# Kernel optimization log

Hardware: AMD Instinct MI355X
Metric: run time of the kernel (lower is better)

The kernel has to match this reference:

```python
import jax, jax.numpy as jnp
import numpy as np

N_NODES = 50000
E_EDGES = 800000
NEG_SLOPE = 0.2  # PyG GATConv LeakyReLU slope
BN_EPS = 1e-5


def _gat(x, src, dst, W, a_s, a_d, b, heads, ch, concat):
    """One GATConv (PyG semantics, eval mode): gather, per-edge attention,
    segment softmax over destination neighborhoods, scatter-add aggregation."""
    n = x.shape[0]
    h = (x @ W).reshape(n, heads, ch)                      # [N,H,C]
    es = jnp.sum(h * a_s, axis=-1)                         # [N,H] alpha_src per node
    ed = jnp.sum(h * a_d, axis=-1)                         # [N,H] alpha_dst per node
    e = jax.nn.leaky_relu(es[src] + ed[dst], NEG_SLOPE)    # [E,H] edge logits
    m = jax.ops.segment_max(e, dst, num_segments=n)        # stable segment softmax
    ex = jnp.exp(e - m[dst])
    den = jax.ops.segment_sum(ex, dst, num_segments=n)
    alpha = ex / den[dst]                                  # [E,H]
    out = jax.ops.segment_sum(h[src] * alpha[:, :, None], dst, num_segments=n)  # [N,H,C]
    out = out.reshape(n, heads * ch) if concat else out.mean(axis=1)
    return out + b


def _bn(x, g, b):
    # eval-mode BatchNorm1d with running_mean=0, running_var=1
    return x * (g / jnp.sqrt(1.0 + BN_EPS)) + b


def setup_inputs() -> dict:
    key = jax.random.key(0)
    k = jax.random.split(key, 24)
    s = 0.1
    inp = {
        "x": jax.random.normal(k[0], (N_NODES, 9), jnp.float32),
        "edge_index": jax.random.randint(k[1], (2, E_EDGES), 0, N_NODES, jnp.int32),
        "W1": jax.random.normal(k[2], (9, 512), jnp.float32) * s,
        "a1s": jax.random.normal(k[3], (8, 64), jnp.float32) * s,
        "a1d": jax.random.normal(k[4], (8, 64), jnp.float32) * s,
        "b1": jax.random.normal(k[5], (512,), jnp.float32) * s,
        "W2": jax.random.normal(k[6], (512, 128), jnp.float32) * s,
        "a2s": jax.random.normal(k[7], (4, 32), jnp.float32) * s,
        "a2d": jax.random.normal(k[8], (4, 32), jnp.float32) * s,
        "b2": jax.random.normal(k[9], (128,), jnp.float32) * s,
        "W3": jax.random.normal(k[10], (128, 32), jnp.float32) * s,
        "a3s": jax.random.normal(k[11], (1, 32), jnp.float32) * s,
        "a3d": jax.random.normal(k[12], (1, 32), jnp.float32) * s,
        "b3": jax.random.normal(k[13], (32,), jnp.float32) * s,
        "g1": jax.random.uniform(k[14], (512,), jnp.float32, 0.5, 1.5),
        "be1": jax.random.normal(k[15], (512,), jnp.float32) * s,
        "g2": jax.random.uniform(k[16], (128,), jnp.float32, 0.5, 1.5),
        "be2": jax.random.normal(k[17], (128,), jnp.float32) * s,
        "g3": jax.random.uniform(k[18], (32,), jnp.float32, 0.5, 1.5),
        "be3": jax.random.normal(k[19], (32,), jnp.float32) * s,
        "Wh": jax.random.normal(k[20], (32, 1), jnp.float32) * s,
        "bh": jax.random.normal(k[21], (1,), jnp.float32) * s,
    }
    return inp


def reference(x, edge_index, W1, a1s, a1d, b1, W2, a2s, a2d, b2,
              W3, a3s, a3d, b3, g1, be1, g2, be2, g3, be3, Wh, bh):
    n = x.shape[0]
    loops = jnp.arange(n, dtype=edge_index.dtype)          # PyG add_self_loops=True
    src = jnp.concatenate([edge_index[0], loops])
    dst = jnp.concatenate([edge_index[1], loops])
    h = _gat(x, src, dst, W1, a1s, a1d, b1, heads=8, ch=64, concat=True)
    h = jax.nn.elu(_bn(h, g1, be1))
    h = _gat(h, src, dst, W2, a2s, a2d, b2, heads=4, ch=32, concat=True)
    h = jax.nn.elu(_bn(h, g2, be2))
    h = _gat(h, src, dst, W3, a3s, a3d, b3, heads=1, ch=32, concat=False)
    h = jax.nn.elu(_bn(h, g3, be3))
    return h @ Wh + bh                                     # [N,1]
```

## Files before the change

### kernel.cpp

```cpp
#include <hip/hip_runtime.h>
#include <hip/hip_bf16.h>
#include <math.h>

#define N_NODES 50000
#define E_EDGES 800000
#define ET (E_EDGES + N_NODES)
#define NBLK_SCAN ((N_NODES + 255) / 256)
#define MPAD 50048
#define NPB_T1 16

typedef __attribute__((ext_vector_type(8))) short bf16x8;
typedef __attribute__((ext_vector_type(4))) float f32x4;
typedef __attribute__((ext_vector_type(8))) _Float16 half8;


__global__ void zero_int_kernel(int* __restrict__ p, int n) {
    int i = blockIdx.x * blockDim.x + threadIdx.x;
    if (i < n) p[i] = 0;
}

__global__ void hist_kernel(const int* __restrict__ ei, int* __restrict__ cnt) {
    int e = blockIdx.x * blockDim.x + threadIdx.x;
    if (e < ET) {
        int d = (e < E_EDGES) ? ei[E_EDGES + e] : (e - E_EDGES);
        atomicAdd(&cnt[d], 1);
    }
}

__global__ void scan1_kernel(const int* __restrict__ cnt, int* __restrict__ rp,
                             int* __restrict__ bsum) {
    __shared__ int s[256];
    int i = blockIdx.x * 256 + threadIdx.x;
    int v = (i < N_NODES) ? cnt[i] : 0;
    s[threadIdx.x] = v;
    __syncthreads();
    for (int off = 1; off < 256; off <<= 1) {
        int t = (threadIdx.x >= off) ? s[threadIdx.x - off] : 0;
        __syncthreads();
        s[threadIdx.x] += t;
        __syncthreads();
    }
    if (i < N_NODES) rp[i + 1] = s[threadIdx.x];
    if (threadIdx.x == 255) bsum[blockIdx.x] = s[255];
}

__global__ void scan2_kernel(int* __restrict__ bsum, int nb) {
    __shared__ int s[256];
    int v = (threadIdx.x < nb) ? bsum[threadIdx.x] : 0;
    s[threadIdx.x] = v;
    __syncthreads();
    for (int off = 1; off < 256; off <<= 1) {
        int t = (threadIdx.x >= off) ? s[threadIdx.x - off] : 0;
        __syncthreads();
        s[threadIdx.x] += t;
        __syncthreads();
    }
    if (threadIdx.x < nb) bsum[threadIdx.x] = (threadIdx.x == 0) ? 0 : s[threadIdx.x - 1];
}

__global__ void scan3_kernel(int* __restrict__ rp, const int* __restrict__ bsum,
                             int* __restrict__ cursor) {
    int i = blockIdx.x * 256 + threadIdx.x;
    if (i == 0) rp[0] = 0;
    if (i < N_NODES) {
        int incl = rp[i + 1] + bsum[i >> 8];
        rp[i + 1] = incl;
        cursor[i] = incl - cursor[i];
    }
}

__global__ void fill_kernel(const int* __restrict__ ei, int* __restrict__ cursor,
                            int* __restrict__ col) {
    int e = blockIdx.x * blockDim.x + threadIdx.x;
    if (e < ET) {
        int s_, d;
        if (e < E_EDGES) { s_ = ei[e]; d = ei[E_EDGES + e]; }
        else             { s_ = e - E_EDGES; d = s_; }
        int p = atomicAdd(&cursor[d], 1);
        col[p] = s_;
    }
}


__global__ void prep_attn1_kernel(const float* __restrict__ W1,
                                  const float* __restrict__ a1s,
                                  const float* __restrict__ a1d,
                                  float* __restrict__ M) {
    int t = threadIdx.x;
    if (t < 144) {
        int which = t / 72, idx = t % 72, k = idx / 8, h = idx % 8;
        const float* a = which ? a1d : a1s;
        float s = 0.f;
        for (int c = 0; c < 64; c++) s += W1[k * 512 + h * 64 + c] * a[h * 64 + c];
        M[t] = s;
    }
}

__global__ void es_ed1_kernel(const float* __restrict__ x, const float* __restrict__ M,
                              float* __restrict__ es, float* __restrict__ ed) {
    int n = blockIdx.x * blockDim.x + threadIdx.x;
    if (n >= N_NODES) return;
    float xr[9];
#pragma unroll
    for (int k = 0; k < 9; k++) xr[k] = x[(size_t)n * 9 + k];
#pragma unroll
    for (int h = 0; h < 8; h++) {
        float s1 = 0.f, s2 = 0.f;
#pragma unroll
        for (int k = 0; k < 9; k++) {
            s1 += xr[k] * M[k * 8 + h];
            s2 += xr[k] * M[72 + k * 8 + h];
        }
        es[(size_t)n * 8 + h] = s1;
        ed[(size_t)n * 8 + h] = s2;
    }
}

__global__ __launch_bounds__(128) void agg1_kernel(const float* __restrict__ x,
        const int* __restrict__ rp, const int* __restrict__ col,
        const float* __restrict__ es, const float* __restrict__ ed,
        float* __restrict__ aggx) {
    __shared__ int   s_src[64];
    __shared__ float s_x[64][9];
    __shared__ float s_es[64][8];
    __shared__ float s_w[8][64];
    __shared__ float s_m[8], s_den[8], s_scale[8], s_ed[8];
    int n = blockIdx.x, tid = threadIdx.x;
    int start = rp[n], end = rp[n + 1];
    if (tid < 8) { s_m[tid] = -INFINITY; s_den[tid] = 0.f; s_ed[tid] = ed[(size_t)n * 8 + tid]; }
    __syncthreads();
    float acc = 0.f;
    int ghh = tid >> 4, glane = tid & 15;
    for (int cs = start; cs < end; cs += 64) {
        int cnt = min(64, end - cs);
        if (tid < cnt) s_src[tid] = col[cs + tid];
        __syncthreads();
        for (int q = tid; q < cnt * 9; q += 128) {
            int e = q / 9, k = q - e * 9;
            s_x[e][k] = x[(size_t)s_src[e] * 9 + k];
        }
        for (int q = tid; q < cnt * 8; q += 128) {
            int e = q >> 3, h = q & 7;
            s_es[e][h] = es[(size_t)s_src[e] * 8 + h];
        }
        __syncthreads();
        float lmax = -INFINITY;
        for (int e = glane; e < cnt; e += 16) {
            float l = s_es[e][ghh] + s_ed[ghh];
            l = (l > 0.f) ? l : 0.2f * l;
            s_w[ghh][e] = l;
            lmax = fmaxf(lmax, l);
        }
#pragma unroll
        for (int off = 8; off > 0; off >>= 1) lmax = fmaxf(lmax, __shfl_xor(lmax, off));
        float mold = s_m[ghh];
        float nm = fmaxf(mold, lmax);
        float fac = __expf(mold - nm);
        float psum = 0.f;
        for (int e = glane; e < cnt; e += 16) {
            float w = __expf(s_w[ghh][e] - nm);
            s_w[ghh][e] = w;
            psum += w;
        }
#pragma unroll
        for (int off = 8; off > 0; off >>= 1) psum += __shfl_xor(psum, off);
        if (glane == 0) { s_den[ghh] = s_den[ghh] * fac + psum; s_m[ghh] = nm; s_scale[ghh] = fac; }
        __syncthreads();
        if (tid < 72) {
            int hh = tid / 9, k = tid - hh * 9;
            float a = acc * s_scale[hh];
            for (int e = 0; e < cnt; e++) a += s_w[hh][e] * s_x[e][k];
            acc = a;
        }
        __syncthreads();
    }
    if (tid < 72) {
        int hh = tid / 9;
        aggx[(size_t)n * 72 + tid] = acc / s_den[hh];
    }
}

__global__ __launch_bounds__(256) void transform1_kernel(const float* __restrict__ aggx,
        const float* __restrict__ W1, const float* __restrict__ b1,
        const float* __restrict__ g1, const float* __restrict__ be1,
        __hip_bfloat16* __restrict__ Ah, __hip_bfloat16* __restrict__ Al) {
    __shared__ float s_a[NPB_T1 * 72];
    int tid = threadIdx.x;
    int n0 = blockIdx.x * NPB_T1;
    int nn = min(NPB_T1, N_NODES - n0);
    for (int q = tid; q < nn * 72; q += 256) s_a[q] = aggx[(size_t)n0 * 72 + q];
    int c0 = tid * 2;
    int hh = c0 >> 6;
    float2 wv[9];
#pragma unroll
    for (int k = 0; k < 9; k++) wv[k] = *(const float2*)&W1[k * 512 + c0];
    float2 bv = *(const float2*)&b1[c0];
    float2 gv = *(const float2*)&g1[c0];
    float2 ev = *(const float2*)&be1[c0];
    float gs0 = gv.x / sqrtf(1.00001f), gs1 = gv.y / sqrtf(1.00001f);
    __syncthreads();
    for (int i = 0; i < nn; i++) {
        const float* ar = &s_a[i * 72 + hh * 9];
        float v0 = bv.x, v1 = bv.y;
#pragma unroll
        for (int k = 0; k < 9; k++) { float a = ar[k]; v0 += a * wv[k].x; v1 += a * wv[k].y; }
        v0 = v0 * gs0 + ev.x;
        v1 = v1 * gs1 + ev.y;
        v0 = (v0 > 0.f) ? v0 : expm1f(v0);
        v1 = (v1 > 0.f) ? v1 : expm1f(v1);
        __hip_bfloat16 h0 = __float2bfloat16(v0), h1 = __float2bfloat16(v1);
        float r0 = v0 - __bfloat162float(h0), r1 = v1 - __bfloat162float(h1);
        size_t base = (size_t)(n0 + i) * 512 + c0;
        __hip_bfloat162 hp; hp.x = h0; hp.y = h1;
        __hip_bfloat162 lp; lp.x = __float2bfloat16(r0); lp.y = __float2bfloat16(r1);
        *(__hip_bfloat162*)&Ah[base] = hp;
        *(__hip_bfloat162*)&Al[base] = lp;
    }
}

__global__ void prep_w2_kernel(const float* __restrict__ W2,
                               __hip_bfloat16* __restrict__ Wh,
                               __hip_bfloat16* __restrict__ Wl) {
    int t = blockIdx.x * 256 + threadIdx.x;
    if (t < 512 * 128) {
        int k = t >> 7, c = t & 127;
        float v = W2[t];
        __hip_bfloat16 hi = __float2bfloat16(v);
        float r = v - __bfloat162float(hi);
        Wh[c * 512 + k] = hi;
        Wl[c * 512 + k] = __float2bfloat16(r);
    }
}


__global__ __launch_bounds__(256) void gemm2_mfma_kernel(
        const __hip_bfloat16* __restrict__ Ah, const __hip_bfloat16* __restrict__ Al,
        const __hip_bfloat16* __restrict__ Wh, const __hip_bfloat16* __restrict__ Wl,
        _Float16* __restrict__ C) {
    __shared__ short lds[32768];
    int tid = threadIdx.x;
    int wv = tid >> 6;
    int lane = tid & 63;
    int lrow = lane & 15, kgrp = lane >> 4;
    int m0 = blockIdx.x * 128;

    f32x4 acc[2][8];
#pragma unroll
    for (int m = 0; m < 2; m++)
#pragma unroll
        for (int n = 0; n < 8; n++) acc[m][n] = (f32x4){0.f, 0.f, 0.f, 0.f};

    for (int kk = 0; kk < 512; kk += 64) {
#pragma unroll
        for (int tI = 0; tI < 4; tI++) {
            const __hip_bfloat16* src = (tI == 0) ? Ah : (tI == 1) ? Al : (tI == 2) ? Wh : Wl;
            int rowBase = (tI < 2) ? m0 : 0;
#pragma unroll
            for (int i = 0; i < 4; i++) {
                int gid = tid + 256 * i;
                int row = gid >> 3, kg = gid & 7;
                bf16x8 v = *(const bf16x8*)(src + (size_t)(rowBase + row) * 512 + kk + kg * 8);
                *(bf16x8*)(lds + tI * 8192 + row * 64 + ((kg ^ (row & 7)) << 3)) = v;
            }
        }
        __syncthreads();
#pragma unroll
        for (int ks = 0; ks < 2; ks++) {
            bf16x8 ah[2], al[2];
#pragma unroll
            for (int m = 0; m < 2; m++) {
                int row = wv * 32 + m * 16 + lrow;
                int kg = ks * 4 + kgrp;
                int so = row * 64 + ((kg ^ (row & 7)) << 3);
                ah[m] = *(const bf16x8*)(lds + so);
                al[m] = *(const bf16x8*)(lds + 8192 + so);
            }
#pragma unroll
            for (int n = 0; n < 8; n++) {
                int colr = n * 16 + lrow;
                int kg = ks * 4 + kgrp;
                int so = colr * 64 + ((kg ^ (colr & 7)) << 3);
                bf16x8 wh = *(const bf16x8*)(lds + 16384 + so);
                bf16x8 wl = *(const bf16x8*)(lds + 24576 + so);
#pragma unroll
                for (int m = 0; m < 2; m++) {
                    acc[m][n] = __builtin_amdgcn_mfma_f32_16x16x32_bf16(ah[m], wh, acc[m][n], 0, 0, 0);
                    acc[m][n] = __builtin_amdgcn_mfma_f32_16x16x32_bf16(al[m], wh, acc[m][n], 0, 0, 0);
                    acc[m][n] = __builtin_amdgcn_mfma_f32_16x16x32_bf16(ah[m], wl, acc[m][n], 0, 0, 0);
                }
            }
        }
        __syncthreads();
    }
#pragma unroll
    for (int m = 0; m < 2; m++) {
#pragma unroll
        for (int n = 0; n < 8; n++) {
#pragma unroll
            for (int r = 0; r < 4; r++) {
                int row = m0 + wv * 32 + m * 16 + (lane >> 4) * 4 + r;
                int colc = n * 16 + (lane & 15);
                if (row < N_NODES) C[(size_t)row * 128 + colc] = (_Float16)acc[m][n][r];
            }
        }
    }
}


template <int TN>
__global__ __launch_bounds__(256) void gemm_h_kernel(
        const float* __restrict__ A, const float* __restrict__ B,
        _Float16* __restrict__ C, int M, int K, int Nd) {
    constexpr int BM = 64, BK = 16;
    constexpr int BN = 32 * TN;
    __shared__ float As[BM * BK];
    __shared__ float Bs[BK * BN];
    int tid = threadIdx.x;
    int m0 = blockIdx.x * BM;
    int n0 = blockIdx.y * BN;
    int tc = tid & 31;
    int tr = tid >> 5;
    float acc[8][TN];
#pragma unroll
    for (int i = 0; i < 8; i++)
#pragma unroll
        for (int j = 0; j < TN; j++) acc[i][j] = 0.f;

    for (int kk = 0; kk < K; kk += BK) {
#pragma unroll
        for (int l = 0; l < (BM * BK) / 256; l++) {
            int e = tid + 256 * l;
            int r = e >> 4, k = e & 15;
            float v = 0.f;
            if (m0 + r < M && kk + k < K) v = A[(size_t)(m0 + r) * K + kk + k];
            As[e] = v;
        }
#pragma unroll
        for (int l = 0; l < (BK * BN) / 256; l++) {
            int e = tid + 256 * l;
            int r = e / BN, c = e % BN;
            float v = 0.f;
            if (kk + r < K) v = B[(size_t)(kk + r) * Nd + n0 + c];
            Bs[e] = v;
        }
        __syncthreads();
#pragma unroll
        for (int k = 0; k < BK; k++) {
            float bv[TN];
#pragma unroll
            for (int j = 0; j < TN; j++) bv[j] = Bs[k * BN + tc * TN + j];
#pragma unroll
            for (int i = 0; i < 8; i++) {
                float a = As[(tr * 8 + i) * BK + k];
#pragma unroll
                for (int j = 0; j < TN; j++) acc[i][j] += a * bv[j];
            }
        }
        __syncthreads();
    }
#pragma unroll
    for (int i = 0; i < 8; i++) {
        int r = m0 + tr * 8 + i;
        if (r < M) {
#pragma unroll
            for (int j = 0; j < TN; j++)
                C[(size_t)r * Nd + n0 + tc * TN + j] = (_Float16)acc[i][j];
        }
    }
}


template <int H, int C>
__global__ void attn_dots_h_kernel(const _Float16* __restrict__ hin,
                                   const float* __restrict__ as_, const float* __restrict__ ad_,
                                   float* __restrict__ es, float* __restrict__ ed) {
    int t = blockIdx.x * blockDim.x + threadIdx.x;
    if (t >= N_NODES * H) return;
    int n = t / H, hh = t % H;
    const half8* row = (const half8*)(hin + (size_t)n * (H * C) + hh * C);
    float s1 = 0.f, s2 = 0.f;
#pragma unroll
    for (int c8 = 0; c8 < C / 8; c8++) {
        half8 v = row[c8];
#pragma unroll
        for (int j = 0; j < 8; j++) {
            float f = (float)v[j];
            s1 += f * as_[hh * C + c8 * 8 + j];
            s2 += f * ad_[hh * C + c8 * 8 + j];
        }
    }
    es[t] = s1;
    ed[t] = s2;
}


template <int H, int C>
__global__ __launch_bounds__((H * C < 64) ? 64 : H * C) void gat_agg_h_kernel(
        const _Float16* __restrict__ hin,
        const int* __restrict__ rp, const int* __restrict__ col,
        const float* __restrict__ es, const float* __restrict__ ed,
        const float* __restrict__ bias, const float* __restrict__ gg,
        const float* __restrict__ bb,
        float* __restrict__ out) {
    constexpr int HC  = H * C;
    constexpr int BLK = (HC < 64) ? 64 : HC;
    constexpr int LPH = (BLK / H > 64) ? 64 : (BLK / H);
    constexpr int RT  = HC / 8;
    constexpr int G   = BLK / RT;
    constexpr int CH  = 64;
    __shared__ int   s_src[CH];
    __shared__ float s_w[H][CH];
    __shared__ float s_red[G][HC];
    __shared__ float s_m[H], s_den[H], s_scale[H], s_ed[H];

    int n = blockIdx.x;
    int tid = threadIdx.x;
    int start = rp[n], end = rp[n + 1];
    if (tid < H) {
        s_m[tid] = -INFINITY;
        s_den[tid] = 0.f;
        s_ed[tid] = ed[(size_t)n * H + tid];
    }
    __syncthreads();

    int ghh = tid / LPH, glane = tid % LPH;
    int g = tid / RT, rl = tid % RT;
    int hh2 = (rl * 8) / C;
    float a0[8], a1[8];
#pragma unroll
    for (int j = 0; j < 8; j++) { a0[j] = 0.f; a1[j] = 0.f; }

    for (int cs = start; cs < end; cs += CH) {
        int cnt = min(CH, end - cs);
        if (tid < cnt) s_src[tid] = col[cs + tid];
        __syncthreads();

        {
            float lmax = -INFINITY;
            for (int e = glane; e < cnt; e += LPH) {
                float l = es[(size_t)s_src[e] * H + ghh] + s_ed[ghh];
                l = (l > 0.f) ? l : 0.2f * l;
                s_w[ghh][e] = l;
                lmax = fmaxf(lmax, l);
            }
#pragma unroll
            for (int off = LPH >> 1; off > 0; off >>= 1)
                lmax = fmaxf(lmax, __shfl_xor(lmax, off));
            float mold = s_m[ghh];
            float nm = fmaxf(mold, lmax);
            float fac = __expf(mold - nm);
            float psum = 0.f;
            for (int e = glane; e < cnt; e += LPH) {
                float w = __expf(s_w[ghh][e] - nm);
                s_w[ghh][e] = w;
                psum += w;
            }
#pragma unroll
            for (int off = LPH >> 1; off > 0; off >>= 1)
                psum += __shfl_xor(psum, off);
            if (glane == 0) {
                s_den[ghh] = s_den[ghh] * fac + psum;
                s_m[ghh] = nm;
                s_scale[ghh] = fac;
            }
        }
        __syncthreads();

        {
            float fac = s_scale[hh2];
#pragma unroll
            for (int j = 0; j < 8; j++) a0[j] *= fac;
            int e = g;
            for (; e + G < cnt; e += 2 * G) {
                float w0 = s_w[hh2][e];
                float w1 = s_w[hh2][e + G];
                half8 v0 = *(const half8*)&hin[(size_t)s_src[e] * HC + rl * 8];
                half8 v1 = *(const half8*)&hin[(size_t)s_src[e + G] * HC + rl * 8];
#pragma unroll
                for (int j = 0; j < 8; j++) a0[j] += w0 * (float)v0[j];
#pragma unroll
                for (int j = 0; j < 8; j++) a1[j] += w1 * (float)v1[j];
            }
            if (e < cnt) {
                float w0 = s_w[hh2][e];
                half8 v0 = *(const half8*)&hin[(size_t)s_src[e] * HC + rl * 8];
#pragma unroll
                for (int j = 0; j < 8; j++) a0[j] += w0 * (float)v0[j];
            }
        }
        __syncthreads();
    }

#pragma unroll
    for (int j = 0; j < 8; j++) s_red[g][rl * 8 + j] = a0[j] + a1[j];
    __syncthreads();
    if (tid < HC) {
        int hh = tid / C;
        float res = 0.f;
#pragma unroll
        for (int q = 0; q < G; q++) res += s_red[q][tid];
        res /= s_den[hh];
        res += bias[tid];
        res = res * (gg[tid] / sqrtf(1.00001f)) + bb[tid];
        res = (res > 0.f) ? res : expm1f(res);
        out[(size_t)n * HC + tid] = res;
    }
}


__global__ void head_kernel(const float* __restrict__ h3, const float* __restrict__ Wh,
                            const float* __restrict__ bh, float* __restrict__ out) {
    int n = blockIdx.x * blockDim.x + threadIdx.x;
    if (n < N_NODES) {
        float s = bh[0];
        const float* row = h3 + (size_t)n * 32;
#pragma unroll
        for (int c = 0; c < 32; c++) s += row[c] * Wh[c];
        out[n] = s;
    }
}


extern "C" void kernel_launch(void* const* d_in, const int* in_sizes, int n_in,
                              void* d_out, int out_size, void* d_ws, size_t ws_size,
                              hipStream_t stream) {
    const float* x   = (const float*)d_in[0];
    const int*   ei  = (const int*)d_in[1];
    const float* W1  = (const float*)d_in[2];
    const float* a1s = (const float*)d_in[3];
    const float* a1d = (const float*)d_in[4];
    const float* b1  = (const float*)d_in[5];
    const float* W2  = (const float*)d_in[6];
    const float* a2s = (const float*)d_in[7];
    const float* a2d = (const float*)d_in[8];
    const float* b2  = (const float*)d_in[9];
    const float* W3  = (const float*)d_in[10];
    const float* a3s = (const float*)d_in[11];
    const float* a3d = (const float*)d_in[12];
    const float* b3  = (const float*)d_in[13];
    const float* g1  = (const float*)d_in[14];
    const float* be1 = (const float*)d_in[15];
    const float* g2  = (const float*)d_in[16];
    const float* be2 = (const float*)d_in[17];
    const float* g3  = (const float*)d_in[18];
    const float* be3 = (const float*)d_in[19];
    const float* Wh  = (const float*)d_in[20];
    const float* bh  = (const float*)d_in[21];
    float* out = (float*)d_out;

    char* ws = (char*)d_ws;
    size_t off = 0;
    auto alloc = [&](size_t bytes) -> void* {
        void* p = ws + off;
        off += (bytes + 255) & ~(size_t)255;
        return p;
    };
    int*   row_ptr = (int*)alloc((N_NODES + 1) * sizeof(int));
    int*   cursor  = (int*)alloc((N_NODES + 1) * sizeof(int));
    int*   bsum    = (int*)alloc(256 * sizeof(int));
    int*   col_src = (int*)alloc((size_t)ET * sizeof(int));
    float* es      = (float*)alloc((size_t)N_NODES * 8 * sizeof(float));
    float* ed      = (float*)alloc((size_t)N_NODES * 8 * sizeof(float));
    float* bufA    = (float*)alloc((size_t)N_NODES * 128 * sizeof(float));
    float* bufB    = (float*)alloc((size_t)N_NODES * 128 * sizeof(float));
    _Float16* h2h  = (_Float16*)alloc((size_t)N_NODES * 128 * sizeof(_Float16));
    _Float16* h3h  = (_Float16*)alloc((size_t)N_NODES * 32 * sizeof(_Float16));
    __hip_bfloat16* Ah   = (__hip_bfloat16*)alloc((size_t)MPAD * 512 * sizeof(__hip_bfloat16));
    __hip_bfloat16* Al   = (__hip_bfloat16*)alloc((size_t)MPAD * 512 * sizeof(__hip_bfloat16));
    __hip_bfloat16* W2Th = (__hip_bfloat16*)alloc((size_t)128 * 512 * sizeof(__hip_bfloat16));
    __hip_bfloat16* W2Tl = (__hip_bfloat16*)alloc((size_t)128 * 512 * sizeof(__hip_bfloat16));
    float* M1 = (float*)(ws + ((ws_size - 1024) & ~(size_t)255));
    float* aggx = bufA;

    zero_int_kernel<<<(N_NODES + 1 + 255) / 256, 256, 0, stream>>>(cursor, N_NODES + 1);
    hist_kernel<<<(ET + 255) / 256, 256, 0, stream>>>(ei, cursor);
    scan1_kernel<<<NBLK_SCAN, 256, 0, stream>>>(cursor, row_ptr, bsum);
    scan2_kernel<<<1, 256, 0, stream>>>(bsum, NBLK_SCAN);
    scan3_kernel<<<NBLK_SCAN, 256, 0, stream>>>(row_ptr, bsum, cursor);
    fill_kernel<<<(ET + 255) / 256, 256, 0, stream>>>(ei, cursor, col_src);

    prep_attn1_kernel<<<1, 256, 0, stream>>>(W1, a1s, a1d, M1);
    es_ed1_kernel<<<(N_NODES + 255) / 256, 256, 0, stream>>>(x, M1, es, ed);
    agg1_kernel<<<N_NODES, 128, 0, stream>>>(x, row_ptr, col_src, es, ed, aggx);
    transform1_kernel<<<(N_NODES + NPB_T1 - 1) / NPB_T1, 256, 0, stream>>>(aggx, W1, b1, g1, be1, Ah, Al);

    prep_w2_kernel<<<256, 256, 0, stream>>>(W2, W2Th, W2Tl);
    gemm2_mfma_kernel<<<MPAD / 128, 256, 0, stream>>>(Ah, Al, W2Th, W2Tl, h2h);
    attn_dots_h_kernel<4, 32><<<(N_NODES * 4 + 255) / 256, 256, 0, stream>>>(h2h, a2s, a2d, es, ed);
    gat_agg_h_kernel<4, 32><<<N_NODES, 128, 0, stream>>>(h2h, row_ptr, col_src, es, ed,
                                                         b2, g2, be2, bufB);

    gemm_h_kernel<1><<<dim3((N_NODES + 63) / 64, 1), 256, 0, stream>>>(bufB, W3, h3h, N_NODES, 128, 32);
    attn_dots_h_kernel<1, 32><<<(N_NODES + 255) / 256, 256, 0, stream>>>(h3h, a3s, a3d, es, ed);
    gat_agg_h_kernel<1, 32><<<N_NODES, 64, 0, stream>>>(h3h, row_ptr, col_src, es, ed,
                                                        b3, g3, be3, bufA);

    head_kernel<<<(N_NODES + 255) / 256, 256, 0, stream>>>(bufA, Wh, bh, out);
}
```

Measured before the change: 431.8 us.

## Fuse layer-2 epilogue with layer-3 GEMM/attention and layer-3 with head

The layer-2 aggregation kernel now applies bias, BN and ELU, multiplies by W3 in-block, and writes fp16 h3 plus the layer-3 attention scalars. The separate GEMM, attention-dot and head kernels are removed. The layer-3 aggregation is specialised to a single head with a wave-wide softmax and folds the final linear head into its epilogue. This removes the fp32 round trip of the 128-wide hidden state and three kernel launches, at the cost of redundant per-node W3 reads and a smaller 64-thread block for layer 2.

```diff
diff --git a/kernel.cpp b/kernel.cpp
--- a/kernel.cpp
+++ b/kernel.cpp
@@ -307,69 +307,6 @@
 }
 
 
-template <int TN>
-__global__ __launch_bounds__(256) void gemm_h_kernel(
-        const float* __restrict__ A, const float* __restrict__ B,
-        _Float16* __restrict__ C, int M, int K, int Nd) {
-    constexpr int BM = 64, BK = 16;
-    constexpr int BN = 32 * TN;
-    __shared__ float As[BM * BK];
-    __shared__ float Bs[BK * BN];
-    int tid = threadIdx.x;
-    int m0 = blockIdx.x * BM;
-    int n0 = blockIdx.y * BN;
-    int tc = tid & 31;
-    int tr = tid >> 5;
-    float acc[8][TN];
-#pragma unroll
-    for (int i = 0; i < 8; i++)
-#pragma unroll
-        for (int j = 0; j < TN; j++) acc[i][j] = 0.f;
-
-    for (int kk = 0; kk < K; kk += BK) {
-#pragma unroll
-        for (int l = 0; l < (BM * BK) / 256; l++) {
-            int e = tid + 256 * l;
-            int r = e >> 4, k = e & 15;
-            float v = 0.f;
-            if (m0 + r < M && kk + k < K) v = A[(size_t)(m0 + r) * K + kk + k];
-            As[e] = v;
-        }
-#pragma unroll
-        for (int l = 0; l < (BK * BN) / 256; l++) {
-            int e = tid + 256 * l;
-            int r = e / BN, c = e % BN;
-            float v = 0.f;
-            if (kk + r < K) v = B[(size_t)(kk + r) * Nd + n0 + c];
-            Bs[e] = v;
-        }
-        __syncthreads();
-#pragma unroll
-        for (int k = 0; k < BK; k++) {
-            float bv[TN];
-#pragma unroll
-            for (int j = 0; j < TN; j++) bv[j] = Bs[k * BN + tc * TN + j];
-#pragma unroll
-            for (int i = 0; i < 8; i++) {
-                float a = As[(tr * 8 + i) * BK + k];
-#pragma unroll
-                for (int j = 0; j < TN; j++) acc[i][j] += a * bv[j];
-            }
-        }
-        __syncthreads();
-    }
-#pragma unroll
-    for (int i = 0; i < 8; i++) {
-        int r = m0 + tr * 8 + i;
-        if (r < M) {
-#pragma unroll
-            for (int j = 0; j < TN; j++)
-                C[(size_t)r * Nd + n0 + tc * TN + j] = (_Float16)acc[i][j];
-        }
-    }
-}
-
-
 template <int H, int C>
 __global__ void attn_dots_h_kernel(const _Float16* __restrict__ hin,
                                    const float* __restrict__ as_, const float* __restrict__ ad_,
@@ -394,38 +331,30 @@
 }
 
 
-template <int H, int C>
-__global__ __launch_bounds__((H * C < 64) ? 64 : H * C) void gat_agg_h_kernel(
+__global__ __launch_bounds__(64) void agg2_fused_kernel(
         const _Float16* __restrict__ hin,
         const int* __restrict__ rp, const int* __restrict__ col,
         const float* __restrict__ es, const float* __restrict__ ed,
-        const float* __restrict__ bias, const float* __restrict__ gg,
-        const float* __restrict__ bb,
-        float* __restrict__ out) {
-    constexpr int HC  = H * C;
-    constexpr int BLK = (HC < 64) ? 64 : HC;
-    constexpr int LPH = (BLK / H > 64) ? 64 : (BLK / H);
-    constexpr int RT  = HC / 8;
-    constexpr int G   = BLK / RT;
-    constexpr int CH  = 64;
+        const float* __restrict__ b2, const float* __restrict__ g2,
+        const float* __restrict__ be2,
+        const float* __restrict__ W3, const float* __restrict__ a3s,
+        const float* __restrict__ a3d,
+        _Float16* __restrict__ h3, float* __restrict__ es3, float* __restrict__ ed3) {
+    constexpr int H = 4, HC = 128, LPH = 16, G = 4, CH = 64;
     __shared__ int   s_src[CH];
     __shared__ float s_w[H][CH];
     __shared__ float s_red[G][HC];
+    __shared__ float s_res[HC];
     __shared__ float s_m[H], s_den[H], s_scale[H], s_ed[H];
 
-    int n = blockIdx.x;
-    int tid = threadIdx.x;
+    int n = blockIdx.x, tid = threadIdx.x;
     int start = rp[n], end = rp[n + 1];
-    if (tid < H) {
-        s_m[tid] = -INFINITY;
-        s_den[tid] = 0.f;
-        s_ed[tid] = ed[(size_t)n * H + tid];
-    }
-    __syncthreads();
-
-    int ghh = tid / LPH, glane = tid % LPH;
-    int g = tid / RT, rl = tid % RT;
-    int hh2 = (rl * 8) / C;
+    if (tid < H) { s_m[tid] = -INFINITY; s_den[tid] = 0.f; s_ed[tid] = ed[(size_t)n * H + tid]; }
+    __syncthreads();
+
+    int ghh = tid >> 4, glane = tid & 15;
+    int g = tid >> 4, rl = tid & 15;
+    int hh2 = rl >> 2;
     float a0[8], a1[8];
 #pragma unroll
     for (int j = 0; j < 8; j++) { a0[j] = 0.f; a1[j] = 0.f; }
@@ -444,8 +373,7 @@
                 lmax = fmaxf(lmax, l);
             }
 #pragma unroll
-            for (int off = LPH >> 1; off > 0; off >>= 1)
-                lmax = fmaxf(lmax, __shfl_xor(lmax, off));
+            for (int off = 8; off > 0; off >>= 1) lmax = fmaxf(lmax, __shfl_xor(lmax, off));
             float mold = s_m[ghh];
             float nm = fmaxf(mold, lmax);
             float fac = __expf(mold - nm);
@@ -456,13 +384,8 @@
                 psum += w;
             }
 #pragma unroll
-            for (int off = LPH >> 1; off > 0; off >>= 1)
-                psum += __shfl_xor(psum, off);
-            if (glane == 0) {
-                s_den[ghh] = s_den[ghh] * fac + psum;
-                s_m[ghh] = nm;
-                s_scale[ghh] = fac;
-            }
+            for (int off = 8; off > 0; off >>= 1) psum += __shfl_xor(psum, off);
+            if (glane == 0) { s_den[ghh] = s_den[ghh] * fac + psum; s_m[ghh] = nm; s_scale[ghh] = fac; }
         }
         __syncthreads();
 
@@ -494,30 +417,131 @@
 #pragma unroll
     for (int j = 0; j < 8; j++) s_red[g][rl * 8 + j] = a0[j] + a1[j];
     __syncthreads();
-    if (tid < HC) {
-        int hh = tid / C;
-        float res = 0.f;
-#pragma unroll
-        for (int q = 0; q < G; q++) res += s_red[q][tid];
-        res /= s_den[hh];
-        res += bias[tid];
-        res = res * (gg[tid] / sqrtf(1.00001f)) + bb[tid];
-        res = (res > 0.f) ? res : expm1f(res);
-        out[(size_t)n * HC + tid] = res;
-    }
-}
-
-
-__global__ void head_kernel(const float* __restrict__ h3, const float* __restrict__ Wh,
-                            const float* __restrict__ bh, float* __restrict__ out) {
-    int n = blockIdx.x * blockDim.x + threadIdx.x;
-    if (n < N_NODES) {
-        float s = bh[0];
-        const float* row = h3 + (size_t)n * 32;
-#pragma unroll
-        for (int c = 0; c < 32; c++) s += row[c] * Wh[c];
-        out[n] = s;
-    }
+
+    const float rsq = 0.99999499f;
+#pragma unroll
+    for (int half = 0; half < 2; half++) {
+        int c = tid + half * 64;
+        float r = s_red[0][c] + s_red[1][c] + s_red[2][c] + s_red[3][c];
+        r /= s_den[c >> 5];
+        r += b2[c];
+        r = r * (g2[c] * rsq) + be2[c];
+        r = (r > 0.f) ? r : expm1f(r);
+        s_res[c] = r;
+    }
+    __syncthreads();
+
+    int halfk = tid >> 5, j = tid & 31;
+    float v = 0.f;
+#pragma unroll 16
+    for (int c = halfk * 64; c < halfk * 64 + 64; c++) v += s_res[c] * W3[c * 32 + j];
+    v += __shfl_xor(v, 32);
+    if (tid < 32) h3[(size_t)n * 32 + j] = (_Float16)v;
+    float p1 = v * a3s[j], p2 = v * a3d[j];
+#pragma unroll
+    for (int off = 16; off > 0; off >>= 1) {
+        p1 += __shfl_xor(p1, off);
+        p2 += __shfl_xor(p2, off);
+    }
+    if (tid == 0) { es3[n] = p1; ed3[n] = p2; }
+}
+
+
+__global__ __launch_bounds__(64) void agg3_fused_kernel(
+        const _Float16* __restrict__ hin,
+        const int* __restrict__ rp, const int* __restrict__ col,
+        const float* __restrict__ es3, const float* __restrict__ ed3,
+        const float* __restrict__ b3, const float* __restrict__ g3,
+        const float* __restrict__ be3,
+        const float* __restrict__ Wh, const float* __restrict__ bh,
+        float* __restrict__ out) {
+    constexpr int G = 16, CH = 64;
+    __shared__ int   s_src[CH];
+    __shared__ float s_w[CH];
+    __shared__ float s_red[G][32];
+    __shared__ float s_m1, s_den1, s_scale1, s_ed1;
+
+    int n = blockIdx.x, tid = threadIdx.x;
+    int start = rp[n], end = rp[n + 1];
+    if (tid == 0) { s_m1 = -INFINITY; s_den1 = 0.f; s_ed1 = ed3[n]; }
+    __syncthreads();
+
+    int g = tid >> 2, rl = tid & 3;
+    float a0[8], a1[8];
+#pragma unroll
+    for (int j = 0; j < 8; j++) { a0[j] = 0.f; a1[j] = 0.f; }
+
+    for (int cs = start; cs < end; cs += CH) {
+        int cnt = min(CH, end - cs);
+        if (tid < cnt) s_src[tid] = col[cs + tid];
+        __syncthreads();
+
+        float lmax = -INFINITY;
+        float l = 0.f;
+        if (tid < cnt) {
+            l = es3[s_src[tid]] + s_ed1;
+            l = (l > 0.f) ? l : 0.2f * l;
+            lmax = l;
+        }
+#pragma unroll
+        for (int off = 32; off > 0; off >>= 1) lmax = fmaxf(lmax, __shfl_xor(lmax, off));
+        float mold = s_m1;
+        float nm = fmaxf(mold, lmax);
+        float fac = __expf(mold - nm);
+        float w = 0.f;
+        if (tid < cnt) {
+            w = __expf(l - nm);
+            s_w[tid] = w;
+        }
+        float psum = w;
+#pragma unroll
+        for (int off = 32; off > 0; off >>= 1) psum += __shfl_xor(psum, off);
+        if (tid == 0) { s_den1 = s_den1 * fac + psum; s_m1 = nm; s_scale1 = fac; }
+        __syncthreads();
+
+        {
+#pragma unroll
+            for (int j = 0; j < 8; j++) a0[j] *= fac;
+            int e = g;
+            for (; e + G < cnt; e += 2 * G) {
+                float w0 = s_w[e];
+                float w1 = s_w[e + G];
+                half8 v0 = *(const half8*)&hin[(size_t)s_src[e] * 32 + rl * 8];
+                half8 v1 = *(const half8*)&hin[(size_t)s_src[e + G] * 32 + rl * 8];
+#pragma unroll
+                for (int j = 0; j < 8; j++) a0[j] += w0 * (float)v0[j];
+#pragma unroll
+                for (int j = 0; j < 8; j++) a1[j] += w1 * (float)v1[j];
+            }
+            if (e < cnt) {
+                float w0 = s_w[e];
+                half8 v0 = *(const half8*)&hin[(size_t)s_src[e] * 32 + rl * 8];
+#pragma unroll
+                for (int j = 0; j < 8; j++) a0[j] += w0 * (float)v0[j];
+            }
+        }
+        __syncthreads();
+    }
+
+#pragma unroll
+    for (int j = 0; j < 8; j++) s_red[g][rl * 8 + j] = a0[j] + a1[j];
+    __syncthreads();
+
+    const float rsq = 0.99999499f;
+    float p = 0.f;
+    if (tid < 32) {
+        float r = 0.f;
+#pragma unroll
+        for (int q = 0; q < G; q++) r += s_red[q][tid];
+        r /= s_den1;
+        r += b3[tid];
+        r = r * (g3[tid] * rsq) + be3[tid];
+        r = (r > 0.f) ? r : expm1f(r);
+        p = r * Wh[tid];
+    }
+#pragma unroll
+    for (int off = 16; off > 0; off >>= 1) p += __shfl_xor(p, off);
+    if (tid == 0) out[n] = p + bh[0];
 }
 
 
@@ -561,8 +585,9 @@
     int*   col_src = (int*)alloc((size_t)ET * sizeof(int));
     float* es      = (float*)alloc((size_t)N_NODES * 8 * sizeof(float));
     float* ed      = (float*)alloc((size_t)N_NODES * 8 * sizeof(float));
-    float* bufA    = (float*)alloc((size_t)N_NODES * 128 * sizeof(float));
-    float* bufB    = (float*)alloc((size_t)N_NODES * 128 * sizeof(float));
+    float* es3     = (float*)alloc((size_t)N_NODES * sizeof(float));
+    float* ed3     = (float*)alloc((size_t)N_NODES * sizeof(float));
+    float* bufA    = (float*)alloc((size_t)N_NODES * 72 * sizeof(float));
     _Float16* h2h  = (_Float16*)alloc((size_t)N_NODES * 128 * sizeof(_Float16));
     _Float16* h3h  = (_Float16*)alloc((size_t)N_NODES * 32 * sizeof(_Float16));
     __hip_bfloat16* Ah   = (__hip_bfloat16*)alloc((size_t)MPAD * 512 * sizeof(__hip_bfloat16));
@@ -587,13 +612,10 @@
     prep_w2_kernel<<<256, 256, 0, stream>>>(W2, W2Th, W2Tl);
     gemm2_mfma_kernel<<<MPAD / 128, 256, 0, stream>>>(Ah, Al, W2Th, W2Tl, h2h);
     attn_dots_h_kernel<4, 32><<<(N_NODES * 4 + 255) / 256, 256, 0, stream>>>(h2h, a2s, a2d, es, ed);
-    gat_agg_h_kernel<4, 32><<<N_NODES, 128, 0, stream>>>(h2h, row_ptr, col_src, es, ed,
-                                                         b2, g2, be2, bufB);
-
-    gemm_h_kernel<1><<<dim3((N_NODES + 63) / 64, 1), 256, 0, stream>>>(bufB, W3, h3h, N_NODES, 128, 32);
-    attn_dots_h_kernel<1, 32><<<(N_NODES + 255) / 256, 256, 0, stream>>>(h3h, a3s, a3d, es, ed);
-    gat_agg_h_kernel<1, 32><<<N_NODES, 64, 0, stream>>>(h3h, row_ptr, col_src, es, ed,
-                                                        b3, g3, be3, bufA);
-
-    head_kernel<<<(N_NODES + 255) / 256, 256, 0, stream>>>(bufA, Wh, bh, out);
-}
+    agg2_fused_kernel<<<N_NODES, 64, 0, stream>>>(h2h, row_ptr, col_src, es, ed,
+                                                  b2, g2, be2, W3, a3s, a3d,
+                                                  h3h, es3, ed3);
+
+    agg3_fused_kernel<<<N_NODES, 64, 0, stream>>>(h3h, row_ptr, col_src, es3, ed3,
+                                                  b3, g3, be3, Wh, bh, out);
+}
```

After: 411.0 us. 1.05x faster.
